# Kernel tuning notes

Hardware: AMD Instinct MI355X
Metric: run time of the kernel (lower is better)

Reference implementation:

```python
import jax, jax.numpy as jnp
import numpy as np

B, C = 8, 8
IMG_H, IMG_W = 512, 1280
MAXDISP = (12, 3, 3)
CH3D = (16, 4, 4)          # channels_3d * growth_rate[i]
LAYERS_3D = 4
BASELINE, FOCAL = 0.2, 320.0
MIN_DEPTH, MAX_DEPTH = 0.1, 100.0


def _conv3d(x, w):
    # x: [B,Cin,D,H,W], w: [Cout,Cin,3,3,3], stride 1, padding 1 -> SAME
    return jax.lax.conv_general_dilated(
        x, w, (1, 1, 1), 'SAME',
        dimension_numbers=('NCDHW', 'OIDHW', 'NCDHW'))


def post_3dconv(cost, w_in, w_mid, w_out):
    # cost: [B,1,D,H,W]; conv->relu stack, final conv back to 1 channel
    x = jax.nn.relu(_conv3d(cost, w_in))
    for k in range(w_mid.shape[0]):
        x = jax.nn.relu(_conv3d(x, w_mid[k]))
    return _conv3d(x, w_out)


def build_volume_2d(fl, fr, maxdisp):
    # L1 cost volume: cost[b,d,h,w] = sum_c |fl[...,w] - fr[...,w-d]|, fr zero-padded left
    Bn, Cn, H, W = fl.shape
    d = jnp.arange(maxdisp)
    src = jnp.arange(W)[None, :] - d[:, None]              # [D,W]
    valid = (src >= 0).astype(fl.dtype)
    fr_s = jnp.take(fr, jnp.clip(src, 0, W - 1), axis=3)   # [B,C,H,D,W]
    fr_s = fr_s * valid[None, None, None]
    cost = jnp.abs(fl[:, :, :, None, :] - fr_s).sum(1)     # [B,H,D,W]
    return jnp.transpose(cost, (0, 2, 1, 3))               # [B,D,H,W]


def build_volume_2d3(fl, fr, maxdisp, disp):
    # residual cost volume around current disparity; warp == horizontal bilinear
    # sampling of fr at x - (disp - shift) with zero padding
    Bn, Cn, H, W = fl.shape
    shifts = jnp.arange(-maxdisp + 1, maxdisp, dtype=fl.dtype)      # [S]
    sd = disp[:, 0][:, None] - shifts[None, :, None, None]          # [B,S,H,W]
    xs = jnp.arange(W, dtype=fl.dtype)[None, None, None, :] - sd   # [B,S,H,W]
    x0 = jnp.floor(xs)
    w1 = xs - x0
    x0i = x0.astype(jnp.int32)

    def sample(xi):
        inb = ((xi >= 0) & (xi <= W - 1)).astype(fl.dtype)
        idx = jnp.clip(xi, 0, W - 1)[:, :, None]                    # [B,S,1,H,W]
        v = jnp.take_along_axis(fr[:, None], idx, axis=-1)          # [B,S,C,H,W]
        return v * inb[:, :, None]

    v = sample(x0i) * (1.0 - w1)[:, :, None] + sample(x0i + 1) * w1[:, :, None]
    return jnp.abs(fl[:, None] - v).sum(2)                          # [B,S,H,W]


def disp_reg(cost, start, end):
    p = jax.nn.softmax(-cost, axis=1)
    d = jnp.arange(start, end, dtype=cost.dtype)[None, :, None, None]
    return jnp.sum(p * d, axis=1, keepdims=True)                    # [B,1,H,W]


def upsample(x, h, w):
    Bn, Cn = x.shape[0], x.shape[1]
    return jax.image.resize(x, (Bn, Cn, h, w), method='bilinear')


def _forward(feats_l, feats_r, params, img_h, img_w):
    pred = []
    for s in range(3):
        fl, fr = feats_l[s], feats_r[s]
        H, W = fl.shape[2], fl.shape[3]
        if s == 0:
            cost = build_volume_2d(fl, fr, MAXDISP[0])
        else:
            wflow = upsample(pred[-1], H, W) * (float(H) / img_h)
            cost = build_volume_2d3(fl, fr, MAXDISP[s], wflow)
        cost = post_3dconv(cost[:, None], *params[s])[:, 0]
        if s == 0:
            d = disp_reg(cost, 0, MAXDISP[0])
        else:
            d = disp_reg(cost, -MAXDISP[s] + 1, MAXDISP[s])
        d = d * (img_h / float(H))
        d_up = upsample(d, img_h, img_w)
        pred.append(d_up if s == 0 else d_up + pred[-1])
    disp = jnp.abs(pred[0])
    depth = jnp.nan_to_num(BASELINE * FOCAL / disp,
                           nan=MAX_DEPTH, posinf=MAX_DEPTH, neginf=MIN_DEPTH)
    depth = jnp.clip(depth, MIN_DEPTH, MAX_DEPTH)
    return pred[0], pred[1], pred[2], depth


def setup_inputs() -> dict:
    key = jax.random.key(0)
    ks = jax.random.split(key, 32)
    ki = iter(range(32))

    def feat(h, w):
        return jax.random.normal(ks[next(ki)], (B, C, h, w), jnp.float32)

    inp = {
        'f_l0': feat(IMG_H // 16, IMG_W // 16), 'f_r0': feat(IMG_H // 16, IMG_W // 16),
        'f_l1': feat(IMG_H // 8, IMG_W // 8),   'f_r1': feat(IMG_H // 8, IMG_W // 8),
        'f_l2': feat(IMG_H // 4, IMG_W // 4),   'f_r2': feat(IMG_H // 4, IMG_W // 4),
    }

    def conv_w(o, i):
        n = 27 * o  # kaiming: 3*3*3*out_channels
        return jax.random.normal(ks[next(ki)], (o, i, 3, 3, 3), jnp.float32) * np.float32(np.sqrt(2.0 / n))

    for s, ch in enumerate(CH3D):
        inp[f'w_in{s}'] = conv_w(ch, 1)
        inp[f'w_mid{s}'] = jnp.stack([conv_w(ch, ch) for _ in range(LAYERS_3D)])
        inp[f'w_out{s}'] = conv_w(1, ch)
    inp['img_h'] = IMG_H
    inp['img_w'] = IMG_W
    return inp


def reference(f_l0, f_r0, f_l1, f_r1, f_l2, f_r2,
              w_in0, w_mid0, w_out0,
              w_in1, w_mid1, w_out1,
              w_in2, w_mid2, w_out2,
              img_h, img_w):
    feats_l = (f_l0, f_l1, f_l2)
    feats_r = (f_r0, f_r1, f_r2)
    params = ((w_in0, w_mid0, w_out0), (w_in1, w_mid1, w_out1), (w_in2, w_mid2, w_out2))
    return _forward(feats_l, feats_r, params, img_h, img_w)
```

## Files before the change

### kernel.cpp

```cpp
#include <hip/hip_runtime.h>
#include <math.h>


#define FULL_H 512
#define FULL_W 1280
#define NB 8
#define NPIX (NB * FULL_H * FULL_W)

__global__ __launch_bounds__(256) void cost0p_k(const float* __restrict__ fl,
                                                const float* __restrict__ fr,
                                                float* __restrict__ costp) {
    const int H = 32, W = 80, D = 12, C = 8;
    const int DZ = 14, HZ = 34, WZ = 88;
    int idx = blockIdx.x * 256 + threadIdx.x;
    int total = NB * D * H * W;
    if (idx >= total) return;
    int w = idx % W; int t = idx / W;
    int h = t % H; t /= H;
    int d = t % D; int b = t / D;
    int src = w - d;
    float acc = 0.f;
    for (int c = 0; c < C; ++c) {
        int base = ((b * C + c) * H + h) * W;
        float flv = fl[base + w];
        float frv = (src >= 0) ? fr[base + src] : 0.f;
        acc += fabsf(flv - frv);
    }
    costp[((b * DZ + (d + 1)) * HZ + (h + 1)) * WZ + (w + 4)] = acc;
}

__global__ __launch_bounds__(256) void costresp_k(const float* __restrict__ fl,
                                                  const float* __restrict__ fr,
                                                  const float* __restrict__ wf,
                                                  float* __restrict__ costp,
                                                  int H, int W, int HZ, int WZ) {
    const int C = 8, S = 5, DZ = 7;
    int idx = blockIdx.x * 256 + threadIdx.x;
    int total = NB * S * H * W;
    if (idx >= total) return;
    int w = idx % W; int t = idx / W;
    int h = t % H; t /= H;
    int s = t % S; int b = t / S;
    float disp  = wf[(b * H + h) * W + w];
    float shift = (float)(s - 2);
    float xs  = (float)w - (disp - shift);
    float x0f = floorf(xs);
    float w1  = xs - x0f;
    float x0fc = fminf(fmaxf(x0f, -2.f), (float)W);
    int x0 = (int)x0fc;
    int x1 = x0 + 1;
    float m0 = (x0 >= 0 && x0 <= W - 1) ? (1.f - w1) : 0.f;
    float m1 = (x1 >= 0 && x1 <= W - 1) ? w1 : 0.f;
    int x0c = min(max(x0, 0), W - 1);
    int x1c = min(max(x1, 0), W - 1);
    float acc = 0.f;
    const float* flb = fl + ((b * C) * H + h) * W;
    const float* frb = fr + ((b * C) * H + h) * W;
    for (int c = 0; c < C; ++c) {
        float v = frb[x0c] * m0 + frb[x1c] * m1;
        acc += fabsf(flb[w] - v);
        flb += H * W;
        frb += H * W;
    }
    costp[((b * DZ + (s + 1)) * HZ + (h + 1)) * WZ + (w + 4)] = acc;
}

template <int CIN, int COUT, int WT, bool RELU, bool PADOUT>
__global__ __launch_bounds__(256) void convp_k(const float* __restrict__ x,
                                               const float* __restrict__ wg,
                                               float* __restrict__ y,
                                               int D, int H, int W,
                                               int DZ, int HZ, int WZ,
                                               int nstrips) {
    __shared__ __align__(16) float wl[CIN * 27 * COUT];
    for (int i = threadIdx.x; i < CIN * 27 * COUT; i += 256) {
        int co = i % COUT; int rest = i / COUT;
        int tap = rest % 27; int ci = rest / 27;
        wl[i] = wg[(co * CIN + ci) * 27 + tap];
    }
    __syncthreads();

    int idx = blockIdx.x * 256 + threadIdx.x;
    if (idx >= nstrips) return;
    const int SW = W / WT;
    int sw = idx % SW; int t = idx / SW;
    int h = t % H; t /= H;
    int d = t % D; int b = t / D;
    const int wcol = sw * WT + 4;
    const int zhs = HZ * WZ;
    const int zcs = DZ * zhs;

    float acc[COUT][WT];
#pragma unroll
    for (int co = 0; co < COUT; ++co)
#pragma unroll
        for (int wt = 0; wt < WT; ++wt) acc[co][wt] = 0.f;

    const float* xb = x + (size_t)b * CIN * zcs + (size_t)d * zhs + (size_t)h * WZ + wcol;

    for (int ci = 0; ci < CIN; ++ci) {
        const float* xc = xb + (size_t)ci * zcs;
#pragma unroll
        for (int kd = 0; kd < 3; ++kd) {
#pragma unroll
            for (int kh = 0; kh < 3; ++kh) {
                const float* row = xc + kd * zhs + kh * WZ;
                float xr[WT + 2];
#pragma unroll
                for (int j = 0; j < WT / 4; ++j) {
                    float4 v = *reinterpret_cast<const float4*>(row + j * 4);
                    xr[1 + j * 4 + 0] = v.x; xr[1 + j * 4 + 1] = v.y;
                    xr[1 + j * 4 + 2] = v.z; xr[1 + j * 4 + 3] = v.w;
                }
                xr[0]      = row[-1];
                xr[WT + 1] = row[WT];
                const int tapbase = ci * 27 + kd * 9 + kh * 3;
#pragma unroll
                for (int kw = 0; kw < 3; ++kw) {
                    const float* wp = &wl[(tapbase + kw) * COUT];
                    if constexpr (COUT == 1) {
                        float wv = wp[0];
#pragma unroll
                        for (int wt = 0; wt < WT; ++wt)
                            acc[0][wt] = fmaf(xr[wt + kw], wv, acc[0][wt]);
                    } else {
                        float4 w4[COUT / 4];
#pragma unroll
                        for (int q = 0; q < COUT / 4; ++q)
                            w4[q] = reinterpret_cast<const float4*>(wp)[q];
#pragma unroll
                        for (int wt = 0; wt < WT; ++wt) {
                            float xv = xr[wt + kw];
#pragma unroll
                            for (int q = 0; q < COUT / 4; ++q) {
                                acc[q * 4 + 0][wt] = fmaf(xv, w4[q].x, acc[q * 4 + 0][wt]);
                                acc[q * 4 + 1][wt] = fmaf(xv, w4[q].y, acc[q * 4 + 1][wt]);
                                acc[q * 4 + 2][wt] = fmaf(xv, w4[q].z, acc[q * 4 + 2][wt]);
                                acc[q * 4 + 3][wt] = fmaf(xv, w4[q].w, acc[q * 4 + 3][wt]);
                            }
                        }
                    }
                }
            }
        }
    }

    if constexpr (PADOUT) {
        float* yb = y + (size_t)b * COUT * zcs + (size_t)(d + 1) * zhs + (size_t)(h + 1) * WZ + wcol;
#pragma unroll
        for (int co = 0; co < COUT; ++co) {
#pragma unroll
            for (int j = 0; j < WT / 4; ++j) {
                float4 v;
                v.x = acc[co][j * 4 + 0]; v.y = acc[co][j * 4 + 1];
                v.z = acc[co][j * 4 + 2]; v.w = acc[co][j * 4 + 3];
                if (RELU) {
                    v.x = fmaxf(v.x, 0.f); v.y = fmaxf(v.y, 0.f);
                    v.z = fmaxf(v.z, 0.f); v.w = fmaxf(v.w, 0.f);
                }
                *reinterpret_cast<float4*>(yb + (size_t)co * zcs + j * 4) = v;
            }
        }
    } else {
        const int chs = D * H * W;
        float* yb = y + (size_t)b * COUT * chs + (d * H + h) * W + sw * WT;
#pragma unroll
        for (int co = 0; co < COUT; ++co) {
#pragma unroll
            for (int j = 0; j < WT / 4; ++j) {
                float4 v;
                v.x = acc[co][j * 4 + 0]; v.y = acc[co][j * 4 + 1];
                v.z = acc[co][j * 4 + 2]; v.w = acc[co][j * 4 + 3];
                if (RELU) {
                    v.x = fmaxf(v.x, 0.f); v.y = fmaxf(v.y, 0.f);
                    v.z = fmaxf(v.z, 0.f); v.w = fmaxf(v.w, 0.f);
                }
                *reinterpret_cast<float4*>(yb + (size_t)co * chs + j * 4) = v;
            }
        }
    }
}

__global__ __launch_bounds__(256) void dispreg_k(const float* __restrict__ cost,
                                                 float* __restrict__ dsm,
                                                 int total, int D, int HW,
                                                 float dstart, float scale) {
    int idx = blockIdx.x * 256 + threadIdx.x;
    if (idx >= total) return;
    int hw = idx % HW; int b = idx / HW;
    const float* c = cost + b * D * HW + hw;
    float m = -1e30f;
    for (int d = 0; d < D; ++d) m = fmaxf(m, -c[d * HW]);
    float s = 0.f, ws = 0.f;
    for (int d = 0; d < D; ++d) {
        float e = expf(-c[d * HW] - m);
        s += e;
        ws = fmaf(e, dstart + (float)d, ws);
    }
    dsm[idx] = ws / s * scale;
}

__global__ __launch_bounds__(256) void upsample_add_k(const float* __restrict__ s,
                                                      int sh, int sw,
                                                      const float* __restrict__ prev,
                                                      float* __restrict__ out,
                                                      float* __restrict__ dep) {
    int idx = blockIdx.x * 256 + threadIdx.x;
    if (idx >= NPIX) return;
    int x = idx % FULL_W; int t = idx / FULL_W;
    int y = t % FULL_H; int b = t / FULL_H;
    float fy = (y + 0.5f) * ((float)sh / FULL_H) - 0.5f;
    float fx = (x + 0.5f) * ((float)sw / FULL_W) - 0.5f;
    int y0 = (int)floorf(fy); float wy = fy - (float)y0;
    int x0 = (int)floorf(fx); float wx = fx - (float)x0;
    int y0c = min(max(y0, 0), sh - 1), y1c = min(max(y0 + 1, 0), sh - 1);
    int x0c = min(max(x0, 0), sw - 1), x1c = min(max(x0 + 1, 0), sw - 1);
    const float* sb = s + b * sh * sw;
    float v00 = sb[y0c * sw + x0c], v01 = sb[y0c * sw + x1c];
    float v10 = sb[y1c * sw + x0c], v11 = sb[y1c * sw + x1c];
    float v = (1.f - wy) * ((1.f - wx) * v00 + wx * v01) +
              wy        * ((1.f - wx) * v10 + wx * v11);
    if (prev) v += prev[idx];
    out[idx] = v;
    if (dep) {
        float p = fabsf(v);
        float d = 64.f / p;
        if (isnan(d)) d = 100.f;
        d = fminf(fmaxf(d, 0.1f), 100.f);
        dep[idx] = d;
    }
}

__global__ __launch_bounds__(256) void wflow_k(const float* __restrict__ pred,
                                               float* __restrict__ wf,
                                               int oh, int ow, int f, float scale) {
    int idx = blockIdx.x * 256 + threadIdx.x;
    int total = NB * oh * ow;
    if (idx >= total) return;
    int ox = idx % ow; int t = idx / ow;
    int oy = t % oh; int b = t / oh;
    float ff = (float)f, invf = 1.f / (float)f;
    float cy = (oy + 0.5f) * ff - 0.5f;
    float cx = (ox + 0.5f) * ff - 0.5f;
    int ylo = max((int)ceilf(cy - ff), 0);
    int yhi = min((int)floorf(cy + ff), FULL_H - 1);
    int xlo = max((int)ceilf(cx - ff), 0);
    int xhi = min((int)floorf(cx + ff), FULL_W - 1);
    const float* pb = pred + b * FULL_H * FULL_W;
    float acc = 0.f, wys = 0.f, wxs = 0.f;
    for (int iy = ylo; iy <= yhi; ++iy) {
        float wy = 1.f - fabsf((float)iy - cy) * invf;
        wys += wy;
        float rowacc = 0.f;
        const float* row = pb + iy * FULL_W;
        for (int ix = xlo; ix <= xhi; ++ix) {
            float wx = 1.f - fabsf((float)ix - cx) * invf;
            rowacc = fmaf(wx, row[ix], rowacc);
        }
        acc = fmaf(wy, rowacc, acc);
    }
    for (int ix = xlo; ix <= xhi; ++ix) wxs += 1.f - fabsf((float)ix - cx) * invf;
    wf[idx] = acc / (wys * wxs) * scale;
}

static inline dim3 g(int n) { return dim3((n + 255) / 256); }

extern "C" void kernel_launch(void* const* d_in, const int* in_sizes, int n_in,
                              void* d_out, int out_size, void* d_ws, size_t ws_size,
                              hipStream_t stream) {
    const float* f_l0  = (const float*)d_in[0];
    const float* f_r0  = (const float*)d_in[1];
    const float* f_l1  = (const float*)d_in[2];
    const float* f_r1  = (const float*)d_in[3];
    const float* f_l2  = (const float*)d_in[4];
    const float* f_r2  = (const float*)d_in[5];
    const float* w_in0  = (const float*)d_in[6];
    const float* w_mid0 = (const float*)d_in[7];
    const float* w_out0 = (const float*)d_in[8];
    const float* w_in1  = (const float*)d_in[9];
    const float* w_mid1 = (const float*)d_in[10];
    const float* w_out1 = (const float*)d_in[11];
    const float* w_in2  = (const float*)d_in[12];
    const float* w_mid2 = (const float*)d_in[13];
    const float* w_out2 = (const float*)d_in[14];

    float* out   = (float*)d_out;
    float* pred0 = out;
    float* pred1 = out + NPIX;
    float* pred2 = out + 2 * NPIX;
    float* depth = out + 3 * NPIX;

    float* ws = (float*)d_ws;
    float* P    = ws;
    float* Q    = ws + 9551360;
    float* CP   = ws + 19102720;
    float* CO   = ws + 21490560;
    float* dsm  = ws + 23128960;
    float* wfl  = ws + 23456640;

    dim3 blk(256);

    {
        const int D = 12, H = 32, W = 80, DZ = 14, HZ = 34, WZ = 88;
        const size_t pcn = (size_t)NB * 16 * DZ * HZ * WZ;
        const size_t cpn = (size_t)NB * DZ * HZ * WZ;
        hipMemsetAsync(P,  0, pcn * 4, stream);
        hipMemsetAsync(Q,  0, pcn * 4, stream);
        hipMemsetAsync(CP, 0, cpn * 4, stream);
        const int total = NB * D * H * W;
        cost0p_k<<<g(total), blk, 0, stream>>>(f_l0, f_r0, CP);
        int ns4 = total / 4;
        int ns8 = total / 8;
        convp_k<1, 16, 4, true, true><<<g(ns4), blk, 0, stream>>>(CP, w_in0, P, D, H, W, DZ, HZ, WZ, ns4);
        const float* src = P; float* dst = Q;
        for (int k = 0; k < 4; ++k) {
            convp_k<16, 16, 4, true, true><<<g(ns4), blk, 0, stream>>>(src, w_mid0 + k * 16 * 16 * 27, dst, D, H, W, DZ, HZ, WZ, ns4);
            const float* nsrc = dst; dst = (float*)src; src = nsrc;
        }
        convp_k<16, 1, 8, false, false><<<g(ns8), blk, 0, stream>>>(src, w_out0, CO, D, H, W, DZ, HZ, WZ, ns8);
        dispreg_k<<<g(NB * H * W), blk, 0, stream>>>(CO, dsm, NB * H * W, D, H * W, 0.f, 16.f);
        upsample_add_k<<<g(NPIX), blk, 0, stream>>>(dsm, H, W, nullptr, pred0, depth);
    }

    {
        const int D = 5, H = 64, W = 160, DZ = 7, HZ = 66, WZ = 168;
        const size_t pcn = (size_t)NB * 4 * DZ * HZ * WZ;
        const size_t cpn = (size_t)NB * DZ * HZ * WZ;
        hipMemsetAsync(P,  0, pcn * 4, stream);
        hipMemsetAsync(Q,  0, pcn * 4, stream);
        hipMemsetAsync(CP, 0, cpn * 4, stream);
        const int total = NB * D * H * W;
        wflow_k<<<g(NB * H * W), blk, 0, stream>>>(pred0, wfl, H, W, 8, 0.125f);
        costresp_k<<<g(total), blk, 0, stream>>>(f_l1, f_r1, wfl, CP, H, W, HZ, WZ);
        int ns4 = total / 4;
        int ns8 = total / 8;
        convp_k<1, 4, 4, true, true><<<g(ns4), blk, 0, stream>>>(CP, w_in1, P, D, H, W, DZ, HZ, WZ, ns4);
        const float* src = P; float* dst = Q;
        for (int k = 0; k < 4; ++k) {
            convp_k<4, 4, 4, true, true><<<g(ns4), blk, 0, stream>>>(src, w_mid1 + k * 4 * 4 * 27, dst, D, H, W, DZ, HZ, WZ, ns4);
            const float* nsrc = dst; dst = (float*)src; src = nsrc;
        }
        convp_k<4, 1, 8, false, false><<<g(ns8), blk, 0, stream>>>(src, w_out1, CO, D, H, W, DZ, HZ, WZ, ns8);
        dispreg_k<<<g(NB * H * W), blk, 0, stream>>>(CO, dsm, NB * H * W, D, H * W, -2.f, 8.f);
        upsample_add_k<<<g(NPIX), blk, 0, stream>>>(dsm, H, W, pred0, pred1, nullptr);
    }

    {
        const int D = 5, H = 128, W = 320, DZ = 7, HZ = 130, WZ = 328;
        const size_t pcn = (size_t)NB * 4 * DZ * HZ * WZ;
        const size_t cpn = (size_t)NB * DZ * HZ * WZ;
        hipMemsetAsync(P,  0, pcn * 4, stream);
        hipMemsetAsync(Q,  0, pcn * 4, stream);
        hipMemsetAsync(CP, 0, cpn * 4, stream);
        const int total = NB * D * H * W;
        wflow_k<<<g(NB * H * W), blk, 0, stream>>>(pred1, wfl, H, W, 4, 0.25f);
        costresp_k<<<g(total), blk, 0, stream>>>(f_l2, f_r2, wfl, CP, H, W, HZ, WZ);
        int ns8 = total / 8;
        convp_k<1, 4, 8, true, true><<<g(ns8), blk, 0, stream>>>(CP, w_in2, P, D, H, W, DZ, HZ, WZ, ns8);
        const float* src = P; float* dst = Q;
        for (int k = 0; k < 4; ++k) {
            convp_k<4, 4, 8, true, true><<<g(ns8), blk, 0, stream>>>(src, w_mid2 + k * 4 * 4 * 27, dst, D, H, W, DZ, HZ, WZ, ns8);
            const float* nsrc = dst; dst = (float*)src; src = nsrc;
        }
        convp_k<4, 1, 8, false, false><<<g(ns8), blk, 0, stream>>>(src, w_out2, CO, D, H, W, DZ, HZ, WZ, ns8);
        dispreg_k<<<g(NB * H * W), blk, 0, stream>>>(CO, dsm, NB * H * W, D, H * W, -2.f, 4.f);
        upsample_add_k<<<g(NPIX), blk, 0, stream>>>(dsm, H, W, pred1, pred2, nullptr);
    }
}
```

Measured before the change: 1.063 ms.

## Double-buffer input rows across channels and shrink conv strip widths

```diff
diff --git a/kernel.cpp b/kernel.cpp
--- a/kernel.cpp
+++ b/kernel.cpp
@@ -65,6 +65,70 @@
     costp[((b * DZ + (s + 1)) * HZ + (h + 1)) * WZ + (w + 4)] = acc;
 }
 
+template <int WT>
+__device__ __forceinline__ void load_rows(const float* __restrict__ xc,
+                                          int zhs, int WZ,
+                                          float* __restrict__ xr ) {
+#pragma unroll
+    for (int kd = 0; kd < 3; ++kd) {
+#pragma unroll
+        for (int kh = 0; kh < 3; ++kh) {
+            const float* row = xc + kd * zhs + kh * WZ;
+            float* r = xr + (kd * 3 + kh) * (WT + 2);
+            if constexpr (WT % 4 == 0) {
+#pragma unroll
+                for (int j = 0; j < WT / 4; ++j) {
+                    float4 v = *reinterpret_cast<const float4*>(row + j * 4);
+                    r[1 + j * 4 + 0] = v.x; r[1 + j * 4 + 1] = v.y;
+                    r[1 + j * 4 + 2] = v.z; r[1 + j * 4 + 3] = v.w;
+                }
+                r[0] = row[-1]; r[WT + 1] = row[WT];
+            } else {
+                r[0] = row[-1]; r[1] = row[0]; r[2] = row[1]; r[3] = row[2];
+            }
+        }
+    }
+}
+
+template <int COUT, int WT>
+__device__ __forceinline__ void fma_ci(const float* __restrict__ xr,
+                                       const float* __restrict__ wlc,
+                                       float* __restrict__ acc ) {
+#pragma unroll
+    for (int kd = 0; kd < 3; ++kd) {
+#pragma unroll
+        for (int kh = 0; kh < 3; ++kh) {
+            const float* r = xr + (kd * 3 + kh) * (WT + 2);
+#pragma unroll
+            for (int kw = 0; kw < 3; ++kw) {
+                const float* wp = wlc + (kd * 9 + kh * 3 + kw) * COUT;
+                if constexpr (COUT == 1) {
+                    float wv = wp[0];
+#pragma unroll
+                    for (int wt = 0; wt < WT; ++wt)
+                        acc[wt] = fmaf(r[wt + kw], wv, acc[wt]);
+                } else {
+                    float4 w4[COUT / 4];
+#pragma unroll
+                    for (int q = 0; q < COUT / 4; ++q)
+                        w4[q] = reinterpret_cast<const float4*>(wp)[q];
+#pragma unroll
+                    for (int wt = 0; wt < WT; ++wt) {
+                        float xv = r[wt + kw];
+#pragma unroll
+                        for (int q = 0; q < COUT / 4; ++q) {
+                            acc[(q * 4 + 0) * WT + wt] = fmaf(xv, w4[q].x, acc[(q * 4 + 0) * WT + wt]);
+                            acc[(q * 4 + 1) * WT + wt] = fmaf(xv, w4[q].y, acc[(q * 4 + 1) * WT + wt]);
+                            acc[(q * 4 + 2) * WT + wt] = fmaf(xv, w4[q].z, acc[(q * 4 + 2) * WT + wt]);
+                            acc[(q * 4 + 3) * WT + wt] = fmaf(xv, w4[q].w, acc[(q * 4 + 3) * WT + wt]);
+                        }
+                    }
+                }
+            }
+        }
+    }
+}
+
 template <int CIN, int COUT, int WT, bool RELU, bool PADOUT>
 __global__ __launch_bounds__(256) void convp_k(const float* __restrict__ x,
                                                const float* __restrict__ wg,
@@ -90,58 +154,27 @@
     const int zhs = HZ * WZ;
     const int zcs = DZ * zhs;
 
-    float acc[COUT][WT];
-#pragma unroll
-    for (int co = 0; co < COUT; ++co)
-#pragma unroll
-        for (int wt = 0; wt < WT; ++wt) acc[co][wt] = 0.f;
-
-    const float* xb = x + (size_t)b * CIN * zcs + (size_t)d * zhs + (size_t)h * WZ + wcol;
-
-    for (int ci = 0; ci < CIN; ++ci) {
-        const float* xc = xb + (size_t)ci * zcs;
-#pragma unroll
-        for (int kd = 0; kd < 3; ++kd) {
-#pragma unroll
-            for (int kh = 0; kh < 3; ++kh) {
-                const float* row = xc + kd * zhs + kh * WZ;
-                float xr[WT + 2];
-#pragma unroll
-                for (int j = 0; j < WT / 4; ++j) {
-                    float4 v = *reinterpret_cast<const float4*>(row + j * 4);
-                    xr[1 + j * 4 + 0] = v.x; xr[1 + j * 4 + 1] = v.y;
-                    xr[1 + j * 4 + 2] = v.z; xr[1 + j * 4 + 3] = v.w;
-                }
-                xr[0]      = row[-1];
-                xr[WT + 1] = row[WT];
-                const int tapbase = ci * 27 + kd * 9 + kh * 3;
-#pragma unroll
-                for (int kw = 0; kw < 3; ++kw) {
-                    const float* wp = &wl[(tapbase + kw) * COUT];
-                    if constexpr (COUT == 1) {
-                        float wv = wp[0];
-#pragma unroll
-                        for (int wt = 0; wt < WT; ++wt)
-                            acc[0][wt] = fmaf(xr[wt + kw], wv, acc[0][wt]);
-                    } else {
-                        float4 w4[COUT / 4];
-#pragma unroll
-                        for (int q = 0; q < COUT / 4; ++q)
-                            w4[q] = reinterpret_cast<const float4*>(wp)[q];
-#pragma unroll
-                        for (int wt = 0; wt < WT; ++wt) {
-                            float xv = xr[wt + kw];
-#pragma unroll
-                            for (int q = 0; q < COUT / 4; ++q) {
-                                acc[q * 4 + 0][wt] = fmaf(xv, w4[q].x, acc[q * 4 + 0][wt]);
-                                acc[q * 4 + 1][wt] = fmaf(xv, w4[q].y, acc[q * 4 + 1][wt]);
-                                acc[q * 4 + 2][wt] = fmaf(xv, w4[q].z, acc[q * 4 + 2][wt]);
-                                acc[q * 4 + 3][wt] = fmaf(xv, w4[q].w, acc[q * 4 + 3][wt]);
-                            }
-                        }
-                    }
-                }
-            }
+    float acc[COUT * WT];
+#pragma unroll
+    for (int i = 0; i < COUT * WT; ++i) acc[i] = 0.f;
+
+    const float* xc = x + (size_t)b * CIN * zcs + (size_t)d * zhs + (size_t)h * WZ + wcol;
+
+    float bufA[9 * (WT + 2)];
+    float bufB[9 * (WT + 2)];
+
+    if constexpr (CIN == 1) {
+        load_rows<WT>(xc, zhs, WZ, bufA);
+        fma_ci<COUT, WT>(bufA, wl, acc);
+    } else {
+        load_rows<WT>(xc, zhs, WZ, bufA);
+        for (int ci = 0; ci < CIN; ci += 2) {
+            load_rows<WT>(xc + zcs, zhs, WZ, bufB);
+            fma_ci<COUT, WT>(bufA, wl + (size_t)ci * 27 * COUT, acc);
+            if (ci + 2 < CIN)
+                load_rows<WT>(xc + 2 * zcs, zhs, WZ, bufA);
+            fma_ci<COUT, WT>(bufB, wl + (size_t)(ci + 1) * 27 * COUT, acc);
+            xc += 2 * zcs;
         }
     }
 
@@ -150,15 +183,10 @@
 #pragma unroll
         for (int co = 0; co < COUT; ++co) {
 #pragma unroll
-            for (int j = 0; j < WT / 4; ++j) {
-                float4 v;
-                v.x = acc[co][j * 4 + 0]; v.y = acc[co][j * 4 + 1];
-                v.z = acc[co][j * 4 + 2]; v.w = acc[co][j * 4 + 3];
-                if (RELU) {
-                    v.x = fmaxf(v.x, 0.f); v.y = fmaxf(v.y, 0.f);
-                    v.z = fmaxf(v.z, 0.f); v.w = fmaxf(v.w, 0.f);
-                }
-                *reinterpret_cast<float4*>(yb + (size_t)co * zcs + j * 4) = v;
+            for (int wt = 0; wt < WT; ++wt) {
+                float v = acc[co * WT + wt];
+                if (RELU) v = fmaxf(v, 0.f);
+                yb[(size_t)co * zcs + wt] = v;
             }
         }
     } else {
@@ -167,15 +195,10 @@
 #pragma unroll
         for (int co = 0; co < COUT; ++co) {
 #pragma unroll
-            for (int j = 0; j < WT / 4; ++j) {
-                float4 v;
-                v.x = acc[co][j * 4 + 0]; v.y = acc[co][j * 4 + 1];
-                v.z = acc[co][j * 4 + 2]; v.w = acc[co][j * 4 + 3];
-                if (RELU) {
-                    v.x = fmaxf(v.x, 0.f); v.y = fmaxf(v.y, 0.f);
-                    v.z = fmaxf(v.z, 0.f); v.w = fmaxf(v.w, 0.f);
-                }
-                *reinterpret_cast<float4*>(yb + (size_t)co * chs + j * 4) = v;
+            for (int wt = 0; wt < WT; ++wt) {
+                float v = acc[co * WT + wt];
+                if (RELU) v = fmaxf(v, 0.f);
+                yb[(size_t)co * chs + wt] = v;
             }
         }
     }
@@ -309,15 +332,15 @@
         hipMemsetAsync(CP, 0, cpn * 4, stream);
         const int total = NB * D * H * W;
         cost0p_k<<<g(total), blk, 0, stream>>>(f_l0, f_r0, CP);
+        int ns2 = total / 2;
         int ns4 = total / 4;
-        int ns8 = total / 8;
-        convp_k<1, 16, 4, true, true><<<g(ns4), blk, 0, stream>>>(CP, w_in0, P, D, H, W, DZ, HZ, WZ, ns4);
+        convp_k<1, 16, 2, true, true><<<g(ns2), blk, 0, stream>>>(CP, w_in0, P, D, H, W, DZ, HZ, WZ, ns2);
         const float* src = P; float* dst = Q;
         for (int k = 0; k < 4; ++k) {
-            convp_k<16, 16, 4, true, true><<<g(ns4), blk, 0, stream>>>(src, w_mid0 + k * 16 * 16 * 27, dst, D, H, W, DZ, HZ, WZ, ns4);
+            convp_k<16, 16, 2, true, true><<<g(ns2), blk, 0, stream>>>(src, w_mid0 + k * 6912, dst, D, H, W, DZ, HZ, WZ, ns2);
             const float* nsrc = dst; dst = (float*)src; src = nsrc;
         }
-        convp_k<16, 1, 8, false, false><<<g(ns8), blk, 0, stream>>>(src, w_out0, CO, D, H, W, DZ, HZ, WZ, ns8);
+        convp_k<16, 1, 4, false, false><<<g(ns4), blk, 0, stream>>>(src, w_out0, CO, D, H, W, DZ, HZ, WZ, ns4);
         dispreg_k<<<g(NB * H * W), blk, 0, stream>>>(CO, dsm, NB * H * W, D, H * W, 0.f, 16.f);
         upsample_add_k<<<g(NPIX), blk, 0, stream>>>(dsm, H, W, nullptr, pred0, depth);
     }
@@ -332,15 +355,15 @@
         const int total = NB * D * H * W;
         wflow_k<<<g(NB * H * W), blk, 0, stream>>>(pred0, wfl, H, W, 8, 0.125f);
         costresp_k<<<g(total), blk, 0, stream>>>(f_l1, f_r1, wfl, CP, H, W, HZ, WZ);
+        int ns2 = total / 2;
         int ns4 = total / 4;
-        int ns8 = total / 8;
-        convp_k<1, 4, 4, true, true><<<g(ns4), blk, 0, stream>>>(CP, w_in1, P, D, H, W, DZ, HZ, WZ, ns4);
+        convp_k<1, 4, 2, true, true><<<g(ns2), blk, 0, stream>>>(CP, w_in1, P, D, H, W, DZ, HZ, WZ, ns2);
         const float* src = P; float* dst = Q;
         for (int k = 0; k < 4; ++k) {
-            convp_k<4, 4, 4, true, true><<<g(ns4), blk, 0, stream>>>(src, w_mid1 + k * 4 * 4 * 27, dst, D, H, W, DZ, HZ, WZ, ns4);
+            convp_k<4, 4, 2, true, true><<<g(ns2), blk, 0, stream>>>(src, w_mid1 + k * 432, dst, D, H, W, DZ, HZ, WZ, ns2);
             const float* nsrc = dst; dst = (float*)src; src = nsrc;
         }
-        convp_k<4, 1, 8, false, false><<<g(ns8), blk, 0, stream>>>(src, w_out1, CO, D, H, W, DZ, HZ, WZ, ns8);
+        convp_k<4, 1, 4, false, false><<<g(ns4), blk, 0, stream>>>(src, w_out1, CO, D, H, W, DZ, HZ, WZ, ns4);
         dispreg_k<<<g(NB * H * W), blk, 0, stream>>>(CO, dsm, NB * H * W, D, H * W, -2.f, 8.f);
         upsample_add_k<<<g(NPIX), blk, 0, stream>>>(dsm, H, W, pred0, pred1, nullptr);
     }
@@ -355,14 +378,14 @@
         const int total = NB * D * H * W;
         wflow_k<<<g(NB * H * W), blk, 0, stream>>>(pred1, wfl, H, W, 4, 0.25f);
         costresp_k<<<g(total), blk, 0, stream>>>(f_l2, f_r2, wfl, CP, H, W, HZ, WZ);
-        int ns8 = total / 8;
-        convp_k<1, 4, 8, true, true><<<g(ns8), blk, 0, stream>>>(CP, w_in2, P, D, H, W, DZ, HZ, WZ, ns8);
+        int ns4 = total / 4;
+        convp_k<1, 4, 4, true, true><<<g(ns4), blk, 0, stream>>>(CP, w_in2, P, D, H, W, DZ, HZ, WZ, ns4);
         const float* src = P; float* dst = Q;
         for (int k = 0; k < 4; ++k) {
-            convp_k<4, 4, 8, true, true><<<g(ns8), blk, 0, stream>>>(src, w_mid2 + k * 4 * 4 * 27, dst, D, H, W, DZ, HZ, WZ, ns8);
+            convp_k<4, 4, 4, true, true><<<g(ns4), blk, 0, stream>>>(src, w_mid2 + k * 432, dst, D, H, W, DZ, HZ, WZ, ns4);
             const float* nsrc = dst; dst = (float*)src; src = nsrc;
         }
-        convp_k<4, 1, 8, false, false><<<g(ns8), blk, 0, stream>>>(src, w_out2, CO, D, H, W, DZ, HZ, WZ, ns8);
+        convp_k<4, 1, 4, false, false><<<g(ns4), blk, 0, stream>>>(src, w_out2, CO, D, H, W, DZ, HZ, WZ, ns4);
         dispreg_k<<<g(NB * H * W), blk, 0, stream>>>(CO, dsm, NB * H * W, D, H * W, -2.f, 4.f);
         upsample_add_k<<<g(NPIX), blk, 0, stream>>>(dsm, H, W, pred1, pred2, nullptr);
     }
```

Result: slower. 1.298 ms (+22.1%).

## Split conv output channels across blocks and double-buffer input-channel loads

Applied to the files above, without the earlier changes.

```diff
diff --git a/kernel.cpp b/kernel.cpp
--- a/kernel.cpp
+++ b/kernel.cpp
@@ -65,118 +65,129 @@
     costp[((b * DZ + (s + 1)) * HZ + (h + 1)) * WZ + (w + 4)] = acc;
 }
 
-template <int CIN, int COUT, int WT, bool RELU, bool PADOUT>
-__global__ __launch_bounds__(256) void convp_k(const float* __restrict__ x,
-                                               const float* __restrict__ wg,
-                                               float* __restrict__ y,
-                                               int D, int H, int W,
-                                               int DZ, int HZ, int WZ,
-                                               int nstrips) {
-    __shared__ __align__(16) float wl[CIN * 27 * COUT];
-    for (int i = threadIdx.x; i < CIN * 27 * COUT; i += 256) {
-        int co = i % COUT; int rest = i / COUT;
+template <int CIN, int COUTT, int COUTS, bool RELU, bool PADOUT>
+__global__ __launch_bounds__(256) void convp4_k(const float* __restrict__ x,
+                                                const float* __restrict__ wg,
+                                                float* __restrict__ y,
+                                                int D, int H, int W,
+                                                int DZ, int HZ, int WZ,
+                                                int nstrips) {
+    constexpr int NSPL = COUTT / COUTS;
+    int cog, bid;
+    if constexpr (NSPL > 1) { cog = blockIdx.x % NSPL; bid = blockIdx.x / NSPL; }
+    else { cog = 0; bid = blockIdx.x; }
+
+    __shared__ __align__(16) float wl[CIN * 27 * COUTS];
+    for (int i = threadIdx.x; i < CIN * 27 * COUTS; i += 256) {
+        int co = i % COUTS; int rest = i / COUTS;
         int tap = rest % 27; int ci = rest / 27;
-        wl[i] = wg[(co * CIN + ci) * 27 + tap];
+        wl[i] = wg[((cog * COUTS + co) * CIN + ci) * 27 + tap];
     }
     __syncthreads();
 
-    int idx = blockIdx.x * 256 + threadIdx.x;
+    int idx = bid * 256 + threadIdx.x;
     if (idx >= nstrips) return;
-    const int SW = W / WT;
+    const int SW = W / 4;
     int sw = idx % SW; int t = idx / SW;
     int h = t % H; t /= H;
     int d = t % D; int b = t / D;
-    const int wcol = sw * WT + 4;
+    const int wcol = sw * 4 + 4;
     const int zhs = HZ * WZ;
     const int zcs = DZ * zhs;
 
-    float acc[COUT][WT];
+    float acc[COUTS][4];
 #pragma unroll
-    for (int co = 0; co < COUT; ++co)
+    for (int co = 0; co < COUTS; ++co)
 #pragma unroll
-        for (int wt = 0; wt < WT; ++wt) acc[co][wt] = 0.f;
+        for (int wt = 0; wt < 4; ++wt) acc[co][wt] = 0.f;
 
     const float* xb = x + (size_t)b * CIN * zcs + (size_t)d * zhs + (size_t)h * WZ + wcol;
 
-    for (int ci = 0; ci < CIN; ++ci) {
-        const float* xc = xb + (size_t)ci * zcs;
+    float A[9][6];
+
+#define LOADCI(BUF, CIDX) do {                                                \
+    const float* xc_ = xb + (size_t)(CIDX) * zcs;                             \
+    _Pragma("unroll")                                                         \
+    for (int r_ = 0; r_ < 9; ++r_) {                                          \
+        const float* row_ = xc_ + (r_ / 3) * zhs + (r_ % 3) * WZ;             \
+        float4 m_ = *reinterpret_cast<const float4*>(row_);                   \
+        BUF[r_][0] = row_[-1];                                                \
+        BUF[r_][1] = m_.x; BUF[r_][2] = m_.y;                                 \
+        BUF[r_][3] = m_.z; BUF[r_][4] = m_.w;                                 \
+        BUF[r_][5] = row_[4];                                                 \
+    } } while (0)
+
+#define FMACI(BUF, CIDX) do {                                                 \
+    const float* wc_ = wl + (size_t)(CIDX) * 27 * COUTS;                      \
+    _Pragma("unroll")                                                         \
+    for (int r_ = 0; r_ < 9; ++r_) {                                          \
+        _Pragma("unroll")                                                     \
+        for (int kw_ = 0; kw_ < 3; ++kw_) {                                   \
+            const float* wp_ = wc_ + (r_ * 3 + kw_) * COUTS;                  \
+            if constexpr (COUTS == 1) {                                       \
+                float wv_ = wp_[0];                                           \
+                _Pragma("unroll")                                             \
+                for (int wt_ = 0; wt_ < 4; ++wt_)                             \
+                    acc[0][wt_] = fmaf(BUF[r_][wt_ + kw_], wv_, acc[0][wt_]); \
+            } else {                                                          \
+                _Pragma("unroll")                                             \
+                for (int q_ = 0; q_ < COUTS / 4; ++q_) {                      \
+                    float4 w4_ = reinterpret_cast<const float4*>(wp_)[q_];    \
+                    _Pragma("unroll")                                         \
+                    for (int wt_ = 0; wt_ < 4; ++wt_) {                       \
+                        float xv_ = BUF[r_][wt_ + kw_];                       \
+                        acc[q_ * 4 + 0][wt_] = fmaf(xv_, w4_.x, acc[q_ * 4 + 0][wt_]); \
+                        acc[q_ * 4 + 1][wt_] = fmaf(xv_, w4_.y, acc[q_ * 4 + 1][wt_]); \
+                        acc[q_ * 4 + 2][wt_] = fmaf(xv_, w4_.z, acc[q_ * 4 + 2][wt_]); \
+                        acc[q_ * 4 + 3][wt_] = fmaf(xv_, w4_.w, acc[q_ * 4 + 3][wt_]); \
+                    }                                                         \
+                }                                                             \
+            }                                                                 \
+        }                                                                     \
+    } } while (0)
+
+    if constexpr (CIN == 1) {
+        LOADCI(A, 0);
+        FMACI(A, 0);
+    } else {
+        float B[9][6];
+        LOADCI(A, 0);
+        for (int ci = 0; ci < CIN; ci += 2) {
+            LOADCI(B, ci + 1);
+            FMACI(A, ci);
+            if (ci + 2 < CIN) LOADCI(A, ci + 2);
+            FMACI(B, ci + 1);
+        }
+    }
+#undef LOADCI
+#undef FMACI
+
+    if constexpr (PADOUT) {
+        float* yb = y + (size_t)b * COUTT * zcs + (size_t)cog * COUTS * zcs
+                  + (size_t)(d + 1) * zhs + (size_t)(h + 1) * WZ + wcol;
 #pragma unroll
-        for (int kd = 0; kd < 3; ++kd) {
-#pragma unroll
-            for (int kh = 0; kh < 3; ++kh) {
-                const float* row = xc + kd * zhs + kh * WZ;
-                float xr[WT + 2];
-#pragma unroll
-                for (int j = 0; j < WT / 4; ++j) {
-                    float4 v = *reinterpret_cast<const float4*>(row + j * 4);
-                    xr[1 + j * 4 + 0] = v.x; xr[1 + j * 4 + 1] = v.y;
-                    xr[1 + j * 4 + 2] = v.z; xr[1 + j * 4 + 3] = v.w;
-                }
-                xr[0]      = row[-1];
-                xr[WT + 1] = row[WT];
-                const int tapbase = ci * 27 + kd * 9 + kh * 3;
-#pragma unroll
-                for (int kw = 0; kw < 3; ++kw) {
-                    const float* wp = &wl[(tapbase + kw) * COUT];
-                    if constexpr (COUT == 1) {
-                        float wv = wp[0];
-#pragma unroll
-                        for (int wt = 0; wt < WT; ++wt)
-                            acc[0][wt] = fmaf(xr[wt + kw], wv, acc[0][wt]);
-                    } else {
-                        float4 w4[COUT / 4];
-#pragma unroll
-                        for (int q = 0; q < COUT / 4; ++q)
-                            w4[q] = reinterpret_cast<const float4*>(wp)[q];
-#pragma unroll
-                        for (int wt = 0; wt < WT; ++wt) {
-                            float xv = xr[wt + kw];
-#pragma unroll
-                            for (int q = 0; q < COUT / 4; ++q) {
-                                acc[q * 4 + 0][wt] = fmaf(xv, w4[q].x, acc[q * 4 + 0][wt]);
-                                acc[q * 4 + 1][wt] = fmaf(xv, w4[q].y, acc[q * 4 + 1][wt]);
-                                acc[q * 4 + 2][wt] = fmaf(xv, w4[q].z, acc[q * 4 + 2][wt]);
-                                acc[q * 4 + 3][wt] = fmaf(xv, w4[q].w, acc[q * 4 + 3][wt]);
-                            }
-                        }
-                    }
-                }
+        for (int co = 0; co < COUTS; ++co) {
+            float4 v;
+            v.x = acc[co][0]; v.y = acc[co][1]; v.z = acc[co][2]; v.w = acc[co][3];
+            if (RELU) {
+                v.x = fmaxf(v.x, 0.f); v.y = fmaxf(v.y, 0.f);
+                v.z = fmaxf(v.z, 0.f); v.w = fmaxf(v.w, 0.f);
             }
-        }
-    }
-
-    if constexpr (PADOUT) {
-        float* yb = y + (size_t)b * COUT * zcs + (size_t)(d + 1) * zhs + (size_t)(h + 1) * WZ + wcol;
-#pragma unroll
-        for (int co = 0; co < COUT; ++co) {
-#pragma unroll
-            for (int j = 0; j < WT / 4; ++j) {
-                float4 v;
-                v.x = acc[co][j * 4 + 0]; v.y = acc[co][j * 4 + 1];
-                v.z = acc[co][j * 4 + 2]; v.w = acc[co][j * 4 + 3];
-                if (RELU) {
-                    v.x = fmaxf(v.x, 0.f); v.y = fmaxf(v.y, 0.f);
-                    v.z = fmaxf(v.z, 0.f); v.w = fmaxf(v.w, 0.f);
-                }
-                *reinterpret_cast<float4*>(yb + (size_t)co * zcs + j * 4) = v;
-            }
+            *reinterpret_cast<float4*>(yb + (size_t)co * zcs) = v;
         }
     } else {
         const int chs = D * H * W;
-        float* yb = y + (size_t)b * COUT * chs + (d * H + h) * W + sw * WT;
+        float* yb = y + (size_t)b * COUTT * chs + (size_t)cog * COUTS * chs
+                  + (d * H + h) * W + sw * 4;
 #pragma unroll
-        for (int co = 0; co < COUT; ++co) {
-#pragma unroll
-            for (int j = 0; j < WT / 4; ++j) {
-                float4 v;
-                v.x = acc[co][j * 4 + 0]; v.y = acc[co][j * 4 + 1];
-                v.z = acc[co][j * 4 + 2]; v.w = acc[co][j * 4 + 3];
-                if (RELU) {
-                    v.x = fmaxf(v.x, 0.f); v.y = fmaxf(v.y, 0.f);
-                    v.z = fmaxf(v.z, 0.f); v.w = fmaxf(v.w, 0.f);
-                }
-                *reinterpret_cast<float4*>(yb + (size_t)co * chs + j * 4) = v;
+        for (int co = 0; co < COUTS; ++co) {
+            float4 v;
+            v.x = acc[co][0]; v.y = acc[co][1]; v.z = acc[co][2]; v.w = acc[co][3];
+            if (RELU) {
+                v.x = fmaxf(v.x, 0.f); v.y = fmaxf(v.y, 0.f);
+                v.z = fmaxf(v.z, 0.f); v.w = fmaxf(v.w, 0.f);
             }
+            *reinterpret_cast<float4*>(yb + (size_t)co * chs) = v;
         }
     }
 }
@@ -264,6 +275,7 @@
 }
 
 static inline dim3 g(int n) { return dim3((n + 255) / 256); }
+static inline dim3 gs(int nstrips, int nspl) { return dim3(((nstrips + 255) / 256) * nspl); }
 
 extern "C" void kernel_launch(void* const* d_in, const int* in_sizes, int n_in,
                               void* d_out, int out_size, void* d_ws, size_t ws_size,
@@ -310,14 +322,13 @@
         const int total = NB * D * H * W;
         cost0p_k<<<g(total), blk, 0, stream>>>(f_l0, f_r0, CP);
         int ns4 = total / 4;
-        int ns8 = total / 8;
-        convp_k<1, 16, 4, true, true><<<g(ns4), blk, 0, stream>>>(CP, w_in0, P, D, H, W, DZ, HZ, WZ, ns4);
+        convp4_k<1, 16, 16, true, true><<<gs(ns4, 1), blk, 0, stream>>>(CP, w_in0, P, D, H, W, DZ, HZ, WZ, ns4);
         const float* src = P; float* dst = Q;
         for (int k = 0; k < 4; ++k) {
-            convp_k<16, 16, 4, true, true><<<g(ns4), blk, 0, stream>>>(src, w_mid0 + k * 16 * 16 * 27, dst, D, H, W, DZ, HZ, WZ, ns4);
+            convp4_k<16, 16, 8, true, true><<<gs(ns4, 2), blk, 0, stream>>>(src, w_mid0 + k * 6912, dst, D, H, W, DZ, HZ, WZ, ns4);
             const float* nsrc = dst; dst = (float*)src; src = nsrc;
         }
-        convp_k<16, 1, 8, false, false><<<g(ns8), blk, 0, stream>>>(src, w_out0, CO, D, H, W, DZ, HZ, WZ, ns8);
+        convp4_k<16, 1, 1, false, false><<<gs(ns4, 1), blk, 0, stream>>>(src, w_out0, CO, D, H, W, DZ, HZ, WZ, ns4);
         dispreg_k<<<g(NB * H * W), blk, 0, stream>>>(CO, dsm, NB * H * W, D, H * W, 0.f, 16.f);
         upsample_add_k<<<g(NPIX), blk, 0, stream>>>(dsm, H, W, nullptr, pred0, depth);
     }
@@ -333,14 +344,13 @@
         wflow_k<<<g(NB * H * W), blk, 0, stream>>>(pred0, wfl, H, W, 8, 0.125f);
         costresp_k<<<g(total), blk, 0, stream>>>(f_l1, f_r1, wfl, CP, H, W, HZ, WZ);
         int ns4 = total / 4;
-        int ns8 = total / 8;
-        convp_k<1, 4, 4, true, true><<<g(ns4), blk, 0, stream>>>(CP, w_in1, P, D, H, W, DZ, HZ, WZ, ns4);
+        convp4_k<1, 4, 4, true, true><<<gs(ns4, 1), blk, 0, stream>>>(CP, w_in1, P, D, H, W, DZ, HZ, WZ, ns4);
         const float* src = P; float* dst = Q;
         for (int k = 0; k < 4; ++k) {
-            convp_k<4, 4, 4, true, true><<<g(ns4), blk, 0, stream>>>(src, w_mid1 + k * 4 * 4 * 27, dst, D, H, W, DZ, HZ, WZ, ns4);
+            convp4_k<4, 4, 4, true, true><<<gs(ns4, 1), blk, 0, stream>>>(src, w_mid1 + k * 432, dst, D, H, W, DZ, HZ, WZ, ns4);
             const float* nsrc = dst; dst = (float*)src; src = nsrc;
         }
-        convp_k<4, 1, 8, false, false><<<g(ns8), blk, 0, stream>>>(src, w_out1, CO, D, H, W, DZ, HZ, WZ, ns8);
+        convp4_k<4, 1, 1, false, false><<<gs(ns4, 1), blk, 0, stream>>>(src, w_out1, CO, D, H, W, DZ, HZ, WZ, ns4);
         dispreg_k<<<g(NB * H * W), blk, 0, stream>>>(CO, dsm, NB * H * W, D, H * W, -2.f, 8.f);
         upsample_add_k<<<g(NPIX), blk, 0, stream>>>(dsm, H, W, pred0, pred1, nullptr);
     }
@@ -355,14 +365,14 @@
         const int total = NB * D * H * W;
         wflow_k<<<g(NB * H * W), blk, 0, stream>>>(pred1, wfl, H, W, 4, 0.25f);
         costresp_k<<<g(total), blk, 0, stream>>>(f_l2, f_r2, wfl, CP, H, W, HZ, WZ);
-        int ns8 = total / 8;
-        convp_k<1, 4, 8, true, true><<<g(ns8), blk, 0, stream>>>(CP, w_in2, P, D, H, W, DZ, HZ, WZ, ns8);
+        int ns4 = total / 4;
+        convp4_k<1, 4, 4, true, true><<<gs(ns4, 1), blk, 0, stream>>>(CP, w_in2, P, D, H, W, DZ, HZ, WZ, ns4);
         const float* src = P; float* dst = Q;
         for (int k = 0; k < 4; ++k) {
-            convp_k<4, 4, 8, true, true><<<g(ns8), blk, 0, stream>>>(src, w_mid2 + k * 4 * 4 * 27, dst, D, H, W, DZ, HZ, WZ, ns8);
+            convp4_k<4, 4, 4, true, true><<<gs(ns4, 1), blk, 0, stream>>>(src, w_mid2 + k * 432, dst, D, H, W, DZ, HZ, WZ, ns4);
             const float* nsrc = dst; dst = (float*)src; src = nsrc;
         }
-        convp_k<4, 1, 8, false, false><<<g(ns8), blk, 0, stream>>>(src, w_out2, CO, D, H, W, DZ, HZ, WZ, ns8);
+        convp4_k<4, 1, 1, false, false><<<gs(ns4, 1), blk, 0, stream>>>(src, w_out2, CO, D, H, W, DZ, HZ, WZ, ns4);
         dispreg_k<<<g(NB * H * W), blk, 0, stream>>>(CO, dsm, NB * H * W, D, H * W, -2.f, 4.f);
         upsample_add_k<<<g(NPIX), blk, 0, stream>>>(dsm, H, W, pred1, pred2, nullptr);
     }
```

Result: faster. 981.9 us (-7.6%).
